# Kernel tuning notes

Hardware: AMD Instinct MI355X
Metric: run time of the kernel (lower is better)

Reference implementation:

```python
import jax, jax.numpy as jnp
import numpy as np

KVOL = 8  # kernel volume of a 2x2x2 transposed conv in 3D


def _tconv(y, T, parent, offset):
    # y: [M, C] coarse features, T: [KVOL, C, D] tconv kernel
    # Each coarse voxel emits KVOL candidate outputs; each existing fine voxel
    # gathers from its unique (parent, offset) pair (gather-GEMM form of
    # MinkowskiConvolutionTranspose with kernel=2, stride=2).
    z = jnp.einsum('mc,kcd->mkd', y, T)  # [M, KVOL, D]
    return z[parent, offset]             # [N_fine, D]


def setup_inputs() -> dict:
    key = jax.random.key(0)
    ks = jax.random.split(key, 12)
    N1, N2, N3 = 400000, 120000, 30000
    C1, C2, C3, D = 64, 128, 256, 128
    inp = {
        'feats1': jax.random.normal(ks[0], (N1, C1), jnp.float32),
        'feats2': jax.random.normal(ks[1], (N2, C2), jnp.float32),
        'feats3': jax.random.normal(ks[2], (N3, C3), jnp.float32),
        'parent1': jax.random.randint(ks[3], (N1,), 0, N2, jnp.int32),
        'offset1': jax.random.randint(ks[4], (N1,), 0, KVOL, jnp.int32),
        'parent2': jax.random.randint(ks[5], (N2,), 0, N3, jnp.int32),
        'offset2': jax.random.randint(ks[6], (N2,), 0, KVOL, jnp.int32),
        'W1': jax.random.normal(ks[7], (C1, D), jnp.float32) * 0.05,
        'W2': jax.random.normal(ks[8], (C2, D), jnp.float32) * 0.05,
        'W3': jax.random.normal(ks[9], (C3, D), jnp.float32) * 0.05,
        'T2': jax.random.normal(ks[10], (KVOL, D, D), jnp.float32) * 0.05,
        'T3': jax.random.normal(ks[11], (KVOL, D, D), jnp.float32) * 0.05,
    }
    return inp


def reference(feats1, feats2, feats3, parent1, offset1, parent2, offset2,
              W1, W2, W3, T2, T3):
    # Top-down FPN merge: start at coarsest level (3), upsample, add skips.
    y = feats3 @ W3                                   # conv1x1['3']
    y = _tconv(y, T3, parent2, offset2) + feats2 @ W2  # tconv['3'] + conv1x1['2']
    y = _tconv(y, T2, parent1, offset1) + feats1 @ W1  # tconv['2'] + conv1x1['1']
    return y  # [N1, out_channels]
```

## Files before the change

### kernel.cpp

```cpp
#include <hip/hip_runtime.h>

typedef __bf16 v8bf __attribute__((ext_vector_type(8)));
typedef float  v4f  __attribute__((ext_vector_type(4)));

__device__ inline unsigned pack_bf16x2(float x, float y) {
    unsigned short a = __builtin_bit_cast(unsigned short, (__bf16)x);
    unsigned short b = __builtin_bit_cast(unsigned short, (__bf16)y);
    return (unsigned)a | ((unsigned)b << 16);
}


__global__ void pack_hist(const float* __restrict__ W1, const float* __restrict__ W2,
                          const float* __restrict__ W3, const float* __restrict__ T2,
                          const float* __restrict__ T3,
                          __bf16* __restrict__ W3T, __bf16* __restrict__ BT3,
                          __bf16* __restrict__ BT2,
                          const int* __restrict__ off1, int n1,
                          const int* __restrict__ off2, int n2, int* __restrict__ ctr) {
    if (blockIdx.x < 1920) {
        int idx = blockIdx.x * 256 + threadIdx.x;
        if (idx < 32768) {
            int c = idx & 255, d = idx >> 8;
            W3T[d * 256 + c] = (__bf16)W3[c * 128 + d];
        } else if (idx < 32768 + 262144) {
            int t = idx - 32768;
            int c = t & 255, rest = t >> 8;
            int d = rest & 127, k = rest >> 7;
            float v = (c < 128) ? T3[((k * 128 + c) * 128) + d] : W2[(c - 128) * 128 + d];
            BT3[t] = (__bf16)v;
        } else if (idx < 32768 + 262144 + 196608) {
            int t = idx - (32768 + 262144);
            int c = t % 192, rest = t / 192;
            int d = rest & 127, k = rest >> 7;
            float v = (c < 128) ? T2[((k * 128 + c) * 128) + d] : W1[(c - 128) * 128 + d];
            BT2[t] = (__bf16)v;
        }
    } else {
        __shared__ int lh[16];
        if (threadIdx.x < 16) lh[threadIdx.x] = 0;
        __syncthreads();
        int total = n1 + n2;
        for (int idx = (blockIdx.x - 1920) * 256 + threadIdx.x; idx < total; idx += 512 * 256) {
            if (idx < n1) atomicAdd(&lh[off1[idx]], 1);
            else          atomicAdd(&lh[8 + off2[idx - n1]], 1);
        }
        __syncthreads();
        if (threadIdx.x < 16) {
            int c = lh[threadIdx.x];
            if (c) atomicAdd(&ctr[threadIdx.x], c);
        }
    }
}

__global__ void scan_kernel(int* ctr) {
    if (threadIdx.x == 0 && blockIdx.x == 0) {
        int s = 0, tb = 0;
        for (int g = 0; g < 8; ++g) {
            ctr[32 + g] = s; ctr[16 + g] = s; ctr[50 + g] = tb;
            s += ctr[g]; tb += (ctr[g] + 63) >> 6;
        }
        ctr[32 + 8] = s; ctr[50 + 8] = tb;
        s = 0; tb = 0;
        for (int g = 0; g < 8; ++g) {
            ctr[41 + g] = s; ctr[24 + g] = s; ctr[59 + g] = tb;
            s += ctr[8 + g]; tb += (ctr[8 + g] + 63) >> 6;
        }
        ctr[41 + 8] = s; ctr[59 + 8] = tb;
    }
}

__global__ void scatter_kernel(const int* __restrict__ off1, int n1, int nb1,
                               const int* __restrict__ off2, int n2,
                               int* __restrict__ ctr, int* __restrict__ perm1,
                               int* __restrict__ perm2) {
    __shared__ int lh[8], gb[8];
    const int* off; int n, base; int* cursor; int* perm;
    if ((int)blockIdx.x < nb1) {
        off = off1; n = n1; base = blockIdx.x * 1024; cursor = ctr + 16; perm = perm1;
    } else {
        off = off2; n = n2; base = (blockIdx.x - nb1) * 1024; cursor = ctr + 24; perm = perm2;
    }
    if (threadIdx.x < 8) lh[threadIdx.x] = 0;
    __syncthreads();
    for (int rr = 0; rr < 4; ++rr) {
        int i = base + rr * 256 + (int)threadIdx.x;
        int o = -1, rank = 0;
        if (i < n) { o = off[i]; rank = atomicAdd(&lh[o], 1); }
        __syncthreads();
        if (threadIdx.x < 8) {
            int c = lh[threadIdx.x];
            gb[threadIdx.x] = c ? atomicAdd(&cursor[threadIdx.x], c) : 0;
        }
        __syncthreads();
        if (o >= 0) perm[gb[o] + rank] = i;
        __syncthreads();
        if (threadIdx.x < 8) lh[threadIdx.x] = 0;
        __syncthreads();
    }
}

template <int K, int CP, int CS, bool GATHER, bool OUT_BF16, int MINW>
__global__ __launch_bounds__(256, MINW) void gemm_k(
    const float* __restrict__ Askip, const __bf16* __restrict__ Aprev,
    const __bf16* __restrict__ BT, const int* __restrict__ perm,
    const int* __restrict__ parent, const int* __restrict__ ctr,
    int gs_off, int tb_off, void* __restrict__ outp, int M) {
    constexpr int LD = K + 8;
    __shared__ __align__(16) __bf16 Al[64 * LD];
    __shared__ int orow[64];

    int g, r0, mcount;
    if constexpr (GATHER) {
        const int* tb = ctr + tb_off;
        int b = blockIdx.x;
        if (b >= tb[8]) return;
        g = 0;
        while (b >= tb[g + 1]) ++g;
        const int* gs = ctr + gs_off;
        r0 = gs[g] + (b - tb[g]) * 64;
        mcount = min(64, gs[g + 1] - r0);
    } else {
        g = 0;
        r0 = blockIdx.x * 64;
        mcount = min(64, M - r0);
    }

    const int tid = threadIdx.x;
    const int lane = tid & 63;
    const int w = tid >> 6;
    const int m = lane & 15;
    const int q = lane >> 4;

    constexpr int KS = K / 32;
    v8bf bfrag[2][KS];
    {
        const __bf16* bbase = BT + ((size_t)g * 128 + w * 32 + m) * K + q * 8;
#pragma unroll
        for (int t = 0; t < 2; ++t)
#pragma unroll
            for (int kk = 0; kk < KS; ++kk)
                bfrag[t][kk] = *(const v8bf*)(bbase + (size_t)t * 16 * K + kk * 32);
    }

    {
        int j = tid >> 2, part = tid & 3;
        if (j < mcount) {
            int i, p = 0;
            if constexpr (GATHER) { i = perm[r0 + j]; p = parent[i]; }
            else { i = r0 + j; }
            if (part == 0) orow[j] = i;
            __bf16* arow = &Al[j * LD];
            if constexpr (CP > 0) {
                const uint4* src = (const uint4*)(Aprev + (size_t)p * CP) + part * (CP / 32);
                uint4* dst = (uint4*)arow + part * (CP / 32);
#pragma unroll
                for (int v = 0; v < CP / 32; ++v) dst[v] = src[v];
            }
            {
                const float4* src = (const float4*)(Askip + (size_t)i * CS) + part * (CS / 16);
                uint4* dst = (uint4*)(arow + CP + part * (CS / 4));
#pragma unroll
                for (int v = 0; v < CS / 16; v += 2) {
                    float4 f0 = src[v], f1 = src[v + 1];
                    uint4 wd;
                    wd.x = pack_bf16x2(f0.x, f0.y);
                    wd.y = pack_bf16x2(f0.z, f0.w);
                    wd.z = pack_bf16x2(f1.x, f1.y);
                    wd.w = pack_bf16x2(f1.z, f1.w);
                    dst[v / 2] = wd;
                }
            }
        }
    }
    __syncthreads();

    v4f acc[4][2] = {};
#pragma unroll
    for (int kk = 0; kk < KS; ++kk) {
#pragma unroll
        for (int rt = 0; rt < 4; ++rt) {
            v8bf a = *(const v8bf*)(&Al[(rt * 16 + m) * LD + q * 8 + kk * 32]);
            acc[rt][0] = __builtin_amdgcn_mfma_f32_16x16x32_bf16(a, bfrag[0][kk], acc[rt][0], 0, 0, 0);
            acc[rt][1] = __builtin_amdgcn_mfma_f32_16x16x32_bf16(a, bfrag[1][kk], acc[rt][1], 0, 0, 0);
        }
    }

#pragma unroll
    for (int rt = 0; rt < 4; ++rt) {
#pragma unroll
        for (int r = 0; r < 4; ++r) {
            int j = rt * 16 + q * 4 + r;
            if (j < mcount) {
                size_t row = (size_t)orow[j] * 128 + w * 32;
                if constexpr (OUT_BF16) {
                    __bf16* out = (__bf16*)outp;
                    out[row + m]      = (__bf16)acc[rt][0][r];
                    out[row + 16 + m] = (__bf16)acc[rt][1][r];
                } else {
                    float* out = (float*)outp;
                    out[row + m]      = acc[rt][0][r];
                    out[row + 16 + m] = acc[rt][1][r];
                }
            }
        }
    }
}

extern "C" void kernel_launch(void* const* d_in, const int* in_sizes, int n_in,
                              void* d_out, int out_size, void* d_ws, size_t ws_size,
                              hipStream_t stream) {
    const float* feats1 = (const float*)d_in[0];
    const float* feats2 = (const float*)d_in[1];
    const float* feats3 = (const float*)d_in[2];
    const int* parent1 = (const int*)d_in[3];
    const int* offset1 = (const int*)d_in[4];
    const int* parent2 = (const int*)d_in[5];
    const int* offset2 = (const int*)d_in[6];
    const float* W1 = (const float*)d_in[7];
    const float* W2 = (const float*)d_in[8];
    const float* W3 = (const float*)d_in[9];
    const float* T2 = (const float*)d_in[10];
    const float* T3 = (const float*)d_in[11];
    const int N1 = in_sizes[0] / 64;
    const int N2 = in_sizes[1] / 128;
    const int N3 = in_sizes[2] / 256;

    char* p = (char*)d_ws;
    auto take = [&](size_t bytes) {
        char* r = p;
        p += (bytes + 255) & ~(size_t)255;
        return r;
    };
    __bf16* y3b = (__bf16*)take((size_t)N3 * 128 * 2);
    __bf16* y2b = (__bf16*)take((size_t)N2 * 128 * 2);
    __bf16* W3T = (__bf16*)take((size_t)32768 * 2);
    __bf16* BT3 = (__bf16*)take((size_t)262144 * 2);
    __bf16* BT2 = (__bf16*)take((size_t)196608 * 2);
    int* perm1 = (int*)take((size_t)N1 * 4);
    int* perm2 = (int*)take((size_t)N2 * 4);
    int* ctr = (int*)take(68 * 4);

    hipMemsetAsync(ctr, 0, 16 * 4, stream);
    pack_hist<<<2432, 256, 0, stream>>>(W1, W2, W3, T2, T3, W3T, BT3, BT2,
                                        offset1, N1, offset2, N2, ctr);
    scan_kernel<<<1, 64, 0, stream>>>(ctr);
    int nb1 = (N1 + 1023) / 1024, nb2 = (N2 + 1023) / 1024;
    scatter_kernel<<<nb1 + nb2, 256, 0, stream>>>(offset1, N1, nb1, offset2, N2, ctr, perm1,
                                                  perm2);
    gemm_k<256, 0, 256, false, true, 3><<<(N3 + 63) / 64, 256, 0, stream>>>(
        feats3, nullptr, W3T, nullptr, nullptr, nullptr, 0, 0, y3b, N3);
    gemm_k<256, 128, 128, true, true, 3><<<(N2 + 63) / 64 + 8, 256, 0, stream>>>(
        feats2, y3b, BT3, perm2, parent2, ctr, 41, 59, y2b, N2);
    gemm_k<192, 128, 64, true, false, 3><<<(N1 + 63) / 64 + 8, 256, 0, stream>>>(
        feats1, y2b, BT2, perm1, parent1, ctr, 32, 50, d_out, N1);
}
```

Measured before the change: 476.8 us.

## Process two row tiles per block with prefetch of second tile's gathers

Replaces the one-tile-per-block gather GEMM for the two tconv levels with a kernel that handles two consecutive 64-row tiles. While the first tile computes, the second tile's parent rows and, optionally, its skip rows are loaded into registers, and the B fragments are reloaded only when the offset group changes. This aims to hide gather latency and amortise B-fragment loads, at the cost of more registers, extra barriers and half as many blocks. The scan kernel also caches the histogram in registers instead of rereading global memory.

```diff
diff --git a/kernel.cpp b/kernel.cpp
--- a/kernel.cpp
+++ b/kernel.cpp
@@ -52,20 +52,25 @@
     }
 }
 
-__global__ void scan_kernel(int* ctr) {
+__global__ void scan_kernel(int* __restrict__ ctr) {
     if (threadIdx.x == 0 && blockIdx.x == 0) {
+        int h[16];
+#pragma unroll
+        for (int x = 0; x < 16; ++x) h[x] = ctr[x];
         int s = 0, tb = 0;
+#pragma unroll
         for (int g = 0; g < 8; ++g) {
             ctr[32 + g] = s; ctr[16 + g] = s; ctr[50 + g] = tb;
-            s += ctr[g]; tb += (ctr[g] + 63) >> 6;
-        }
-        ctr[32 + 8] = s; ctr[50 + 8] = tb;
+            s += h[g]; tb += (h[g] + 63) >> 6;
+        }
+        ctr[40] = s; ctr[58] = tb;
         s = 0; tb = 0;
+#pragma unroll
         for (int g = 0; g < 8; ++g) {
             ctr[41 + g] = s; ctr[24 + g] = s; ctr[59 + g] = tb;
-            s += ctr[8 + g]; tb += (ctr[8 + g] + 63) >> 6;
-        }
-        ctr[41 + 8] = s; ctr[59 + 8] = tb;
+            s += h[8 + g]; tb += (h[8 + g] + 63) >> 6;
+        }
+        ctr[49] = s; ctr[67] = tb;
     }
 }
 
@@ -204,6 +209,171 @@
             }
         }
     }
+}
+
+template <int K, int CP, int CS, bool OUT_BF16, bool PREF_SKIP>
+__global__ __launch_bounds__(256, 3) void gemm_pair(
+    const float* __restrict__ Askip, const __bf16* __restrict__ Aprev,
+    const __bf16* __restrict__ BT, const int* __restrict__ perm,
+    const int* __restrict__ parent, const int* __restrict__ ctr,
+    int gs_off, int tb_off, void* __restrict__ outp) {
+    constexpr int LD = K + 8;
+    constexpr int KS = K / 32;
+    constexpr int NAP = CP / 32;
+    constexpr int NSK = CS / 16;
+    __shared__ __align__(16) __bf16 Al[64 * LD];
+    __shared__ int orow[64];
+
+    int tb[9], gs[9];
+#pragma unroll
+    for (int x = 0; x < 9; ++x) tb[x] = ctr[tb_off + x];
+#pragma unroll
+    for (int x = 0; x < 9; ++x) gs[x] = ctr[gs_off + x];
+
+    const int total = tb[8];
+    const int t0 = (int)blockIdx.x * 2;
+    const int t1 = t0 + 1;
+    if (t0 >= total) return;
+    const bool has1 = (t1 < total);
+
+    auto locate = [&](int t, int& g, int& r0, int& mc) {
+        int gg = 0, tbg = tb[0], gsg = gs[0], gse = gs[1];
+#pragma unroll
+        for (int x = 1; x < 8; ++x) {
+            if (t >= tb[x]) { gg = x; tbg = tb[x]; gsg = gs[x]; gse = gs[x + 1]; }
+        }
+        g = gg; r0 = gsg + (t - tbg) * 64; mc = min(64, gse - r0);
+    };
+    int g0, r00, mc0, g1 = 0, r01 = 0, mc1 = 0;
+    locate(t0, g0, r00, mc0);
+    if (has1) locate(t1, g1, r01, mc1);
+
+    const int tid = (int)threadIdx.x;
+    const int lane = tid & 63;
+    const int w = tid >> 6;
+    const int m = lane & 15;
+    const int q = lane >> 4;
+    const int j = tid >> 2;
+    const int part = tid & 3;
+
+    int i0 = -1, p0 = 0, i1 = -1, p1 = 0;
+    if (j < mc0) i0 = perm[r00 + j];
+    if (has1 && j < mc1) i1 = perm[r01 + j];
+    if (j < mc0) p0 = parent[i0];
+    if (has1 && j < mc1) p1 = parent[i1];
+
+    v8bf bfrag[2][KS];
+    {
+        const __bf16* bbase = BT + ((size_t)g0 * 128 + w * 32 + m) * K + q * 8;
+#pragma unroll
+        for (int t = 0; t < 2; ++t)
+#pragma unroll
+            for (int kk = 0; kk < KS; ++kk)
+                bfrag[t][kk] = *(const v8bf*)(bbase + (size_t)t * 16 * K + kk * 32);
+    }
+
+    uint4 apr[NAP];
+    float4 skr[NSK];
+    if (j < mc0) {
+        const uint4* asrc = (const uint4*)(Aprev + (size_t)p0 * CP) + part * NAP;
+#pragma unroll
+        for (int v = 0; v < NAP; ++v) apr[v] = asrc[v];
+        const float4* ssrc = (const float4*)(Askip + (size_t)i0 * CS) + part * NSK;
+#pragma unroll
+        for (int v = 0; v < NSK; ++v) skr[v] = ssrc[v];
+    }
+
+    auto stage = [&](int mc, int i) {
+        if (j < mc) {
+            if (part == 0) orow[j] = i;
+            __bf16* arow = &Al[j * LD];
+            uint4* dst = (uint4*)arow + part * NAP;
+#pragma unroll
+            for (int v = 0; v < NAP; ++v) dst[v] = apr[v];
+            uint4* sdst = (uint4*)(arow + CP + part * (CS / 4));
+#pragma unroll
+            for (int v = 0; v < NSK; v += 2) {
+                uint4 wd;
+                wd.x = pack_bf16x2(skr[v].x, skr[v].y);
+                wd.y = pack_bf16x2(skr[v].z, skr[v].w);
+                wd.z = pack_bf16x2(skr[v + 1].x, skr[v + 1].y);
+                wd.w = pack_bf16x2(skr[v + 1].z, skr[v + 1].w);
+                sdst[v / 2] = wd;
+            }
+        }
+    };
+
+    auto compute_and_store = [&](int mc) {
+        v4f acc[4][2] = {};
+#pragma unroll
+        for (int kk = 0; kk < KS; ++kk) {
+#pragma unroll
+            for (int rt = 0; rt < 4; ++rt) {
+                v8bf a = *(const v8bf*)(&Al[(rt * 16 + m) * LD + q * 8 + kk * 32]);
+                acc[rt][0] = __builtin_amdgcn_mfma_f32_16x16x32_bf16(a, bfrag[0][kk], acc[rt][0], 0, 0, 0);
+                acc[rt][1] = __builtin_amdgcn_mfma_f32_16x16x32_bf16(a, bfrag[1][kk], acc[rt][1], 0, 0, 0);
+            }
+        }
+#pragma unroll
+        for (int rt = 0; rt < 4; ++rt) {
+#pragma unroll
+            for (int r = 0; r < 4; ++r) {
+                int jj = rt * 16 + q * 4 + r;
+                if (jj < mc) {
+                    size_t row = (size_t)orow[jj] * 128 + w * 32;
+                    if constexpr (OUT_BF16) {
+                        __bf16* out = (__bf16*)outp;
+                        out[row + m]      = (__bf16)acc[rt][0][r];
+                        out[row + 16 + m] = (__bf16)acc[rt][1][r];
+                    } else {
+                        float* out = (float*)outp;
+                        out[row + m]      = acc[rt][0][r];
+                        out[row + 16 + m] = acc[rt][1][r];
+                    }
+                }
+            }
+        }
+    };
+
+    stage(mc0, i0);
+    __syncthreads();
+
+    if (has1 && j < mc1) {
+        const uint4* asrc = (const uint4*)(Aprev + (size_t)p1 * CP) + part * NAP;
+#pragma unroll
+        for (int v = 0; v < NAP; ++v) apr[v] = asrc[v];
+        if constexpr (PREF_SKIP) {
+            const float4* ssrc = (const float4*)(Askip + (size_t)i1 * CS) + part * NSK;
+#pragma unroll
+            for (int v = 0; v < NSK; ++v) skr[v] = ssrc[v];
+        }
+    }
+
+    compute_and_store(mc0);
+
+    if (!has1) return;
+
+    if constexpr (!PREF_SKIP) {
+        if (j < mc1) {
+            const float4* ssrc = (const float4*)(Askip + (size_t)i1 * CS) + part * NSK;
+#pragma unroll
+            for (int v = 0; v < NSK; ++v) skr[v] = ssrc[v];
+        }
+    }
+    if (g1 != g0) {
+        const __bf16* bbase = BT + ((size_t)g1 * 128 + w * 32 + m) * K + q * 8;
+#pragma unroll
+        for (int t = 0; t < 2; ++t)
+#pragma unroll
+            for (int kk = 0; kk < KS; ++kk)
+                bfrag[t][kk] = *(const v8bf*)(bbase + (size_t)t * 16 * K + kk * 32);
+    }
+    __syncthreads();
+
+    stage(mc1, i1);
+    __syncthreads();
+
+    compute_and_store(mc1);
 }
 
 extern "C" void kernel_launch(void* const* d_in, const int* in_sizes, int n_in,
@@ -249,8 +419,10 @@
                                                   perm2);
     gemm_k<256, 0, 256, false, true, 3><<<(N3 + 63) / 64, 256, 0, stream>>>(
         feats3, nullptr, W3T, nullptr, nullptr, nullptr, 0, 0, y3b, N3);
-    gemm_k<256, 128, 128, true, true, 3><<<(N2 + 63) / 64 + 8, 256, 0, stream>>>(
-        feats2, y3b, BT3, perm2, parent2, ctr, 41, 59, y2b, N2);
-    gemm_k<192, 128, 64, true, false, 3><<<(N1 + 63) / 64 + 8, 256, 0, stream>>>(
-        feats1, y2b, BT2, perm1, parent1, ctr, 32, 50, d_out, N1);
-}
+    int nt2 = (N2 + 63) / 64 + 8;
+    gemm_pair<256, 128, 128, true, false><<<(nt2 + 1) / 2, 256, 0, stream>>>(
+        feats2, y3b, BT3, perm2, parent2, ctr, 41, 59, y2b);
+    int nt1 = (N1 + 63) / 64 + 8;
+    gemm_pair<192, 128, 64, false, true><<<(nt1 + 1) / 2, 256, 0, stream>>>(
+        feats1, y2b, BT2, perm1, parent1, ctr, 32, 50, d_out);
+}
```

New measurement: 503.6 us. +5.6%, slower.
